# Performance work log

Hardware: AMD Instinct MI355X
Metric: run time of the kernel (lower is better)

The kernel has to match this reference:

```python
import jax, jax.numpy as jnp
import numpy as np

B, N, V, H = 8, 2048, 256, 1024
EPS = 1e-5
NEG = -1e9


def _layernorm(x, g, b):
    m = jnp.mean(x, axis=-1, keepdims=True)
    v = jnp.mean((x - m) ** 2, axis=-1, keepdims=True)
    return (x - m) / jnp.sqrt(v + EPS) * g + b


def setup_inputs() -> dict:
    key = jax.random.key(0)
    ks = jax.random.split(key, 10)
    tril = jnp.tril(jnp.ones((N, N), jnp.float32))
    return {
        "h": jax.random.normal(ks[0], (B, N, V), jnp.float32),
        "mask_one": tril,                      # keep causal entries
        "mask_zero": NEG * (1.0 - tril),       # -inf-ish above diagonal
        "ln_attn_g": jnp.ones((V,), jnp.float32),
        "ln_attn_b": jnp.zeros((V,), jnp.float32),
        "ln_mlp_g": jnp.ones((V,), jnp.float32),
        "ln_mlp_b": jnp.zeros((V,), jnp.float32),
        "wv": jax.random.normal(ks[1], (V,), jnp.float32),
        "wv_bos": jax.random.normal(ks[2], (V,), jnp.float32),
        "wo_w": jax.random.normal(ks[3], (V, V), jnp.float32) / np.sqrt(V),
        "qk_bos": jax.random.normal(ks[4], (V,), jnp.float32),
        "qk_previous": jax.random.normal(ks[5], (V,), jnp.float32),
        "qk_direction": jnp.ones((V,), jnp.float32),  # middel_layer=False, frozen
        "w1": jax.random.normal(ks[6], (H, V), jnp.float32) / np.sqrt(V),
        "w2": jax.random.normal(ks[7], (V, H), jnp.float32) / np.sqrt(H),
    }


def reference(h, mask_one, mask_zero, ln_attn_g, ln_attn_b, ln_mlp_g, ln_mlp_b,
              wv, wv_bos, wo_w, qk_bos, qk_previous, qk_direction, w1, w2):
    b, n, v = h.shape
    # mask blends LayerNorm only into row 0 (BOS position)
    attn_input = h.at[:, 0, :].set(_layernorm(h[:, 0, :], ln_attn_g, ln_attn_b))
    # value states: diag(wv) on positions 1.., wo(wv_bos) at position 0
    values = attn_input[:, 1:, :] * wv                      # [B, N-1, V]
    v_bos = wo_w @ wv_bos                                   # Linear(bias=False)
    values = jnp.concatenate(
        [jnp.broadcast_to(v_bos, (b, 1, v)), values], axis=1)  # [B, N, V]
    # sparse QK logits: column 0 term + sub-diagonal term, densified then masked
    col0 = (attn_input @ qk_bos) * (attn_input[:, 0, :] @ qk_direction)[:, None]  # [B, N]
    d = attn_input @ qk_previous                            # [B, N]
    qk = jnp.zeros((b, n, n), h.dtype).at[:, :, 0].add(col0)
    idx = jnp.arange(1, n)
    qk = qk.at[:, idx, idx - 1].add(d[:, 1:])               # row r, col r-1 = d[:, r]
    qk = qk * mask_one + mask_zero
    attn_out = jax.nn.softmax(qk, axis=-1) @ values         # [B, N, V]
    # FFN branch with its own BOS-only LayerNorm blend
    mlp_input = h.at[:, 0, :].set(_layernorm(h[:, 0, :], ln_mlp_g, ln_mlp_b))
    mlp_out = jax.nn.relu(mlp_input @ w1.T) @ w2.T          # [B, N, V]
    return attn_out + mlp_out
```

## Files before the change

### kernel.cpp

```cpp
#include <hip/hip_runtime.h>
#include <hip/hip_bf16.h>

#define BB 8
#define NN 2048
#define VV 256
#define HH 1024
#define CHK 64
#define RPC 32
constexpr float EPS = 1e-5f;

typedef __attribute__((ext_vector_type(4))) float floatx4;
typedef __attribute__((ext_vector_type(8))) short short8;

__device__ __forceinline__ void load_lds16(const void* g, void* l) {
    __builtin_amdgcn_global_load_lds((const __attribute__((address_space(1))) void*)g,
                                     (__attribute__((address_space(3))) void*)l, 16, 0, 0);
}
__device__ __forceinline__ float bf16s_to_f(short s) {
    unsigned u = ((unsigned)(unsigned short)s) << 16;
    return __builtin_bit_cast(float, u);
}

__global__ void prep_kernel(const float* __restrict__ h,
                            const float* __restrict__ g_attn, const float* __restrict__ b_attn,
                            const float* __restrict__ g_mlp,  const float* __restrict__ b_mlp,
                            const float* __restrict__ qk_dir,
                            const float* __restrict__ wo_w,  const float* __restrict__ wv_bos,
                            float* __restrict__ attn_row0, float* __restrict__ mlp_row0,
                            float* __restrict__ v_bos, float* __restrict__ sum0)
{
    int t = threadIdx.x;
    __shared__ float red[VV];
    if (blockIdx.x < BB) {
        int b = blockIdx.x;
        float x = h[(size_t)b * NN * VV + t];
        red[t] = x; __syncthreads();
        for (int s = 128; s > 0; s >>= 1) { if (t < s) red[t] += red[t + s]; __syncthreads(); }
        float m = red[0] * (1.0f / VV); __syncthreads();
        float xc = x - m;
        red[t] = xc * xc; __syncthreads();
        for (int s = 128; s > 0; s >>= 1) { if (t < s) red[t] += red[t + s]; __syncthreads(); }
        float var = red[0] * (1.0f / VV); __syncthreads();
        float inv = 1.0f / sqrtf(var + EPS);
        float an = xc * inv * g_attn[t] + b_attn[t];
        float mn = xc * inv * g_mlp[t] + b_mlp[t];
        attn_row0[b * VV + t] = an;
        mlp_row0[b * VV + t]  = mn;
        red[t] = an * qk_dir[t]; __syncthreads();
        for (int s = 128; s > 0; s >>= 1) { if (t < s) red[t] += red[t + s]; __syncthreads(); }
        if (t == 0) sum0[b] = red[0];
    } else {
        const float4* wp = reinterpret_cast<const float4*>(wo_w + (size_t)t * VV);
        const float4* vp = reinterpret_cast<const float4*>(wv_bos);
        float acc = 0.f;
        for (int j = 0; j < VV / 4; ++j) {
            float4 a = wp[j], b = vp[j];
            acc += a.x * b.x + a.y * b.y + a.z * b.z + a.w * b.w;
        }
        v_bos[t] = acc;
    }
}

__global__ __launch_bounds__(256) void scan_qkw_cvt_kernel(
    const float* __restrict__ h, const float* __restrict__ mlp_row0,
    const float* __restrict__ wv,
    const float* __restrict__ qk_bos, const float* __restrict__ qk_prev,
    const float* __restrict__ sum0,
    short* __restrict__ Xb,
    float* __restrict__ w0, float* __restrict__ wprev, float* __restrict__ wz,
    float* __restrict__ chunkSum)
{
    __shared__ float lds[4][VV];
    int wave = threadIdx.x >> 6, lane = threadIdx.x & 63;
    int b = blockIdx.x / CHK, c = blockIdx.x % CHK;
    int r0 = c * RPC + wave * 8;
    float4 wv4 = reinterpret_cast<const float4*>(wv)[lane];
    float4 qb4 = reinterpret_cast<const float4*>(qk_bos)[lane];
    float4 qp4 = reinterpret_cast<const float4*>(qk_prev)[lane];
    float s0b = sum0[b];
    float4 vsum = {0.f, 0.f, 0.f, 0.f};
#pragma unroll
    for (int rr = 0; rr < 8; ++rr) {
        int r = r0 + rr;
        size_t base = ((size_t)b * NN + r) * VV;
        float4 x = *reinterpret_cast<const float4*>(h + base + lane * 4);
        float4 xs = x;
        if (r == 0) xs = *reinterpret_cast<const float4*>(mlp_row0 + b * VV + lane * 4);
        __hip_bfloat16 c0 = __float2bfloat16(xs.x), c1 = __float2bfloat16(xs.y),
                       c2 = __float2bfloat16(xs.z), c3 = __float2bfloat16(xs.w);
        short4 pk;
        pk.x = *reinterpret_cast<short*>(&c0);
        pk.y = *reinterpret_cast<short*>(&c1);
        pk.z = *reinterpret_cast<short*>(&c2);
        pk.w = *reinterpret_cast<short*>(&c3);
        *reinterpret_cast<short4*>(Xb + base + lane * 4) = pk;
        if (r != 0) {
            vsum.x += bf16s_to_f(pk.x) * wv4.x; vsum.y += bf16s_to_f(pk.y) * wv4.y;
            vsum.z += bf16s_to_f(pk.z) * wv4.z; vsum.w += bf16s_to_f(pk.w) * wv4.w;
        }
        float s1 = x.x * qb4.x + x.y * qb4.y + x.z * qb4.z + x.w * qb4.w;
        float s2 = x.x * qp4.x + x.y * qp4.y + x.z * qp4.z + x.w * qp4.w;
        for (int off = 32; off > 0; off >>= 1) {
            s1 += __shfl_down(s1, off);
            s2 += __shfl_down(s2, off);
        }
        if (lane == 0) {
            int gid = b * NN + r;
            float W0, WP, WZ;
            if (r == 0) { W0 = 1.f; WP = 0.f; WZ = 0.f; }
            else if (r == 1) {
                float a = s1 * s0b + s2;
                float m = fmaxf(a, 0.f);
                float ea = expf(a - m), ez = expf(-m);
                float Z = ea + ez;
                W0 = ea / Z; WZ = ez / Z; WP = WZ;
            } else {
                float a = s1 * s0b;
                float m = fmaxf(fmaxf(a, s2), 0.f);
                float ea = expf(a - m), ed = expf(s2 - m), ez = expf(-m);
                float Z = ea + ed + (float)(r - 1) * ez;
                W0 = ea / Z; WP = ed / Z; WZ = ez / Z;
            }
            w0[gid] = W0; wprev[gid] = WP; wz[gid] = WZ;
        }
    }
    reinterpret_cast<float4*>(lds[wave])[lane] = vsum;
    __syncthreads();
    int v = threadIdx.x;
    chunkSum[((size_t)b * CHK + c) * VV + v] = lds[0][v] + lds[1][v] + lds[2][v] + lds[3][v];
}

__global__ void chunkscan_kernel(float* __restrict__ chunkSum)
{
    int b = blockIdx.x, v = threadIdx.x;
    float vals[CHK];
#pragma unroll
    for (int c = 0; c < CHK; ++c) vals[c] = chunkSum[(b * CHK + c) * VV + v];
    float run = 0.f;
#pragma unroll
    for (int c = 0; c < CHK; ++c) { float t = vals[c]; vals[c] = run; run += t; }
#pragma unroll
    for (int c = 0; c < CHK; ++c) chunkSum[(b * CHK + c) * VV + v] = vals[c];
}

__global__ __launch_bounds__(128) void attn_kernel(
    const short* __restrict__ Xb, const float* __restrict__ wv,
    const float* __restrict__ v_bos,
    const float* __restrict__ w0, const float* __restrict__ wprev,
    const float* __restrict__ wz, const float* __restrict__ chunkSum,
    float* __restrict__ out)
{
    int b = blockIdx.x / CHK, c = blockIdx.x % CHK;
    int v = threadIdx.x * 2;
    float2 wv2 = *reinterpret_cast<const float2*>(wv + v);
    float2 vb2 = *reinterpret_cast<const float2*>(v_bos + v);
    float2 S = *reinterpret_cast<const float2*>(chunkSum + (b * CHK + c) * VV + v);
    int r0 = c * RPC;
    float2 prev = {0.f, 0.f};
    if (r0 > 0) {
        short2 p = *reinterpret_cast<const short2*>(Xb + ((size_t)b * NN + r0 - 1) * VV + v);
        prev.x = bf16s_to_f(p.x) * wv2.x; prev.y = bf16s_to_f(p.y) * wv2.y;
    }
    for (int r = r0; r < r0 + RPC; ++r) {
        size_t idx = ((size_t)b * NN + r) * VV + v;
        float2 o;
        if (r == 0) {
            o = vb2;
            prev.x = 0.f; prev.y = 0.f;
        } else {
            short2 xv = *reinterpret_cast<const short2*>(Xb + idx);
            float2 val;
            val.x = bf16s_to_f(xv.x) * wv2.x; val.y = bf16s_to_f(xv.y) * wv2.y;
            S.x += val.x; S.y += val.y;
            int wi = b * NN + r;
            float W0 = w0[wi], WD = wprev[wi] - wz[wi], WZ = wz[wi];
            o.x = W0 * vb2.x + WD * prev.x + WZ * S.x;
            o.y = W0 * vb2.y + WD * prev.y + WZ * S.y;
            prev = val;
        }
        *reinterpret_cast<float2*>(out + idx) = o;
    }
}

__global__ void cvt_w_kernel(const float* __restrict__ w1, const float* __restrict__ w2,
                             __hip_bfloat16* __restrict__ w1b, __hip_bfloat16* __restrict__ w2b)
{
    int i = (blockIdx.x * blockDim.x + threadIdx.x) * 4;
    const float* src;
    __hip_bfloat16* dst;
    if (i < HH * VV) { src = w1 + i; dst = w1b + i; }
    else             { src = w2 + (i - HH * VV); dst = w2b + (i - HH * VV); }
    float4 x = *reinterpret_cast<const float4*>(src);
    dst[0] = __float2bfloat16(x.x);
    dst[1] = __float2bfloat16(x.y);
    dst[2] = __float2bfloat16(x.z);
    dst[3] = __float2bfloat16(x.w);
}

__global__ __launch_bounds__(512) void mlp_fused3(const short* __restrict__ Xb,
                                                  const short* __restrict__ w1b,
                                                  const short* __restrict__ w2b,
                                                  float* __restrict__ out)
{
    __shared__ __align__(16) short sW1[2][64 * 256];
    __shared__ __align__(16) short sW2[2][256 * 64];
    __shared__ __align__(16) short sY[64 * 64];
    int wave = threadIdx.x >> 6, lane = threadIdx.x & 63;
    int wm = wave >> 2, wn = wave & 3;
    int ra = lane & 15, q = lane >> 4;
    int m0 = blockIdx.x * 64;

    short8 xf[8][2];
#pragma unroll
    for (int ks = 0; ks < 8; ++ks)
#pragma unroll
        for (int i = 0; i < 2; ++i)
            xf[ks][i] = *reinterpret_cast<const short8*>(
                Xb + (size_t)(m0 + wm * 32 + i * 16 + ra) * VV + ks * 32 + q * 8);

    floatx4 oacc[2][4];
#pragma unroll
    for (int i = 0; i < 2; ++i)
#pragma unroll
        for (int j = 0; j < 4; ++j) oacc[i][j] = floatx4{0.f, 0.f, 0.f, 0.f};

    auto stage = [&](int hc, int buf) {
#pragma unroll
        for (int it = 0; it < 4; ++it) {
            int g = wave * 4 + it;
            int n = g * 2 + (lane >> 5);
            int slot = lane & 31;
            load_lds16(w1b + (size_t)(hc * 64 + n) * VV + (slot ^ (n & 7)) * 8,
                       &sW1[buf][g * 512]);
        }
#pragma unroll
        for (int it = 0; it < 4; ++it) {
            int g = wave * 4 + it;
            int v = g * 8 + (lane >> 3);
            int slot = lane & 7;
            load_lds16(w2b + (size_t)v * HH + hc * 64 + (slot ^ (v & 7)) * 8,
                       &sW2[buf][g * 512]);
        }
    };

    stage(0, 0);
    for (int hc = 0; hc < 16; ++hc) {
        int p = hc & 1;
        __syncthreads();
        if (hc < 15) stage(hc + 1, p ^ 1);

        floatx4 yacc[2];
        yacc[0] = floatx4{0.f, 0.f, 0.f, 0.f};
        yacc[1] = floatx4{0.f, 0.f, 0.f, 0.f};
        int nb = wn * 16 + ra;
#pragma unroll
        for (int ks = 0; ks < 8; ++ks) {
            short8 bfr = *reinterpret_cast<const short8*>(
                &sW1[p][nb * 256 + (((ks * 4 + q) ^ (ra & 7)) * 8)]);
#pragma unroll
            for (int i = 0; i < 2; ++i)
                yacc[i] = __builtin_amdgcn_mfma_f32_16x16x32_bf16(xf[ks][i], bfr, yacc[i], 0, 0, 0);
        }
#pragma unroll
        for (int i = 0; i < 2; ++i)
#pragma unroll
            for (int reg = 0; reg < 4; ++reg) {
                int m = wm * 32 + i * 16 + q * 4 + reg;
                int ke = wn * 16 + ra;
                __hip_bfloat16 hb = __float2bfloat16(fmaxf(yacc[i][reg], 0.f));
                sY[m * 64 + (((ke >> 3) ^ (m & 7)) * 8) + (ke & 7)] =
                    *reinterpret_cast<short*>(&hb);
            }
        __syncthreads();

#pragma unroll
        for (int kk = 0; kk < 2; ++kk) {
            short8 a2[2];
#pragma unroll
            for (int i = 0; i < 2; ++i) {
                int m = wm * 32 + i * 16 + ra;
                a2[i] = *reinterpret_cast<const short8*>(
                    &sY[m * 64 + (((kk * 4 + q) ^ (ra & 7)) * 8)]);
            }
#pragma unroll
            for (int j = 0; j < 4; ++j) {
                int v = wn * 64 + j * 16 + ra;
                short8 b2 = *reinterpret_cast<const short8*>(
                    &sW2[p][v * 64 + (((kk * 4 + q) ^ (ra & 7)) * 8)]);
#pragma unroll
                for (int i = 0; i < 2; ++i)
                    oacc[i][j] = __builtin_amdgcn_mfma_f32_16x16x32_bf16(a2[i], b2, oacc[i][j], 0, 0, 0);
            }
        }
    }

#pragma unroll
    for (int i = 0; i < 2; ++i)
#pragma unroll
        for (int j = 0; j < 4; ++j)
#pragma unroll
            for (int reg = 0; reg < 4; ++reg) {
                int row = m0 + wm * 32 + i * 16 + q * 4 + reg;
                int col = wn * 64 + j * 16 + ra;
                out[(size_t)row * VV + col] += oacc[i][j][reg];
            }
}

extern "C" void kernel_launch(void* const* d_in, const int* in_sizes, int n_in,
                              void* d_out, int out_size, void* d_ws, size_t ws_size,
                              hipStream_t stream)
{
    const float* h        = (const float*)d_in[0];
    const float* ln_attn_g = (const float*)d_in[3];
    const float* ln_attn_b = (const float*)d_in[4];
    const float* ln_mlp_g  = (const float*)d_in[5];
    const float* ln_mlp_b  = (const float*)d_in[6];
    const float* wv        = (const float*)d_in[7];
    const float* wv_bos    = (const float*)d_in[8];
    const float* wo_w      = (const float*)d_in[9];
    const float* qk_bos    = (const float*)d_in[10];
    const float* qk_prev   = (const float*)d_in[11];
    const float* qk_dir    = (const float*)d_in[12];
    const float* w1        = (const float*)d_in[13];
    const float* w2        = (const float*)d_in[14];
    float* out = (float*)d_out;

    float* attn_row0 = (float*)d_ws;
    float* mlp_row0  = attn_row0 + BB * VV;
    float* v_bos     = mlp_row0 + BB * VV;
    float* sum0      = v_bos + VV;
    float* w0        = sum0 + 8;
    float* wprev     = w0 + BB * NN;
    float* wzz       = wprev + BB * NN;
    float* chunkSum  = wzz + BB * NN;
    short* Xb            = (short*)(chunkSum + BB * CHK * VV);
    __hip_bfloat16* w1b  = (__hip_bfloat16*)(Xb + (size_t)BB * NN * VV);
    __hip_bfloat16* w2b  = w1b + HH * VV;

    prep_kernel<<<BB + 1, 256, 0, stream>>>(h, ln_attn_g, ln_attn_b, ln_mlp_g, ln_mlp_b,
                                            qk_dir, wo_w, wv_bos,
                                            attn_row0, mlp_row0, v_bos, sum0);
    cvt_w_kernel<<<(2 * HH * VV / 4) / 256, 256, 0, stream>>>(w1, w2, w1b, w2b);
    scan_qkw_cvt_kernel<<<BB * CHK, 256, 0, stream>>>(h, mlp_row0, wv, qk_bos, qk_prev,
                                                      sum0, Xb, w0, wprev, wzz, chunkSum);
    chunkscan_kernel<<<BB, 256, 0, stream>>>(chunkSum);
    attn_kernel<<<BB * CHK, 128, 0, stream>>>(Xb, wv, v_bos, w0, wprev, wzz, chunkSum, out);
    mlp_fused3<<<256, 512, 0, stream>>>(Xb, (const short*)w1b, (const short*)w2b, out);
}
```

Baseline: 172.3 us.

## Merge weight conversion into prep, drop chunk scan kernel, restructure MLP to 4 waves

Weight bf16 conversion is folded into the prep kernel as extra blocks, and the separate chunk-scan kernel is removed: each attention block now sums its preceding chunk totals itself. The MLP kernel moves from 8 waves to 4 waves per block, with each wave covering all 64 rows and doubling its accumulator tiles. The next-chunk weight staging is issued after the first GEMM's barrier instead of before it. These cut launch count and per-block synchronisation, at the cost of redundant prefix reads in the attention kernel and higher register pressure in the MLP.

```diff
diff --git a/kernel.cpp b/kernel.cpp
--- a/kernel.cpp
+++ b/kernel.cpp
@@ -21,15 +21,30 @@
     return __builtin_bit_cast(float, u);
 }
 
-__global__ void prep_kernel(const float* __restrict__ h,
-                            const float* __restrict__ g_attn, const float* __restrict__ b_attn,
-                            const float* __restrict__ g_mlp,  const float* __restrict__ b_mlp,
-                            const float* __restrict__ qk_dir,
-                            const float* __restrict__ wo_w,  const float* __restrict__ wv_bos,
-                            float* __restrict__ attn_row0, float* __restrict__ mlp_row0,
-                            float* __restrict__ v_bos, float* __restrict__ sum0)
+__global__ void prep_cvt_kernel(const float* __restrict__ h,
+                                const float* __restrict__ g_attn, const float* __restrict__ b_attn,
+                                const float* __restrict__ g_mlp,  const float* __restrict__ b_mlp,
+                                const float* __restrict__ qk_dir,
+                                const float* __restrict__ wo_w,  const float* __restrict__ wv_bos,
+                                const float* __restrict__ w1, const float* __restrict__ w2,
+                                float* __restrict__ attn_row0, float* __restrict__ mlp_row0,
+                                float* __restrict__ v_bos, float* __restrict__ sum0,
+                                __hip_bfloat16* __restrict__ w1b, __hip_bfloat16* __restrict__ w2b)
 {
     int t = threadIdx.x;
+    if (blockIdx.x > BB) {
+        int i = ((blockIdx.x - BB - 1) * 256 + t) * 4;
+        const float* src;
+        __hip_bfloat16* dst;
+        if (i < HH * VV) { src = w1 + i; dst = w1b + i; }
+        else             { src = w2 + (i - HH * VV); dst = w2b + (i - HH * VV); }
+        float4 x = *reinterpret_cast<const float4*>(src);
+        dst[0] = __float2bfloat16(x.x);
+        dst[1] = __float2bfloat16(x.y);
+        dst[2] = __float2bfloat16(x.z);
+        dst[3] = __float2bfloat16(x.w);
+        return;
+    }
     __shared__ float red[VV];
     if (blockIdx.x < BB) {
         int b = blockIdx.x;
@@ -130,19 +145,6 @@
     chunkSum[((size_t)b * CHK + c) * VV + v] = lds[0][v] + lds[1][v] + lds[2][v] + lds[3][v];
 }
 
-__global__ void chunkscan_kernel(float* __restrict__ chunkSum)
-{
-    int b = blockIdx.x, v = threadIdx.x;
-    float vals[CHK];
-#pragma unroll
-    for (int c = 0; c < CHK; ++c) vals[c] = chunkSum[(b * CHK + c) * VV + v];
-    float run = 0.f;
-#pragma unroll
-    for (int c = 0; c < CHK; ++c) { float t = vals[c]; vals[c] = run; run += t; }
-#pragma unroll
-    for (int c = 0; c < CHK; ++c) chunkSum[(b * CHK + c) * VV + v] = vals[c];
-}
-
 __global__ __launch_bounds__(128) void attn_kernel(
     const short* __restrict__ Xb, const float* __restrict__ wv,
     const float* __restrict__ v_bos,
@@ -154,7 +156,11 @@
     int v = threadIdx.x * 2;
     float2 wv2 = *reinterpret_cast<const float2*>(wv + v);
     float2 vb2 = *reinterpret_cast<const float2*>(v_bos + v);
-    float2 S = *reinterpret_cast<const float2*>(chunkSum + (b * CHK + c) * VV + v);
+    float2 S = {0.f, 0.f};
+    for (int cc = 0; cc < c; ++cc) {
+        float2 t = *reinterpret_cast<const float2*>(chunkSum + (b * CHK + cc) * VV + v);
+        S.x += t.x; S.y += t.y;
+    }
     int r0 = c * RPC;
     float2 prev = {0.f, 0.f};
     if (r0 > 0) {
@@ -182,63 +188,47 @@
     }
 }
 
-__global__ void cvt_w_kernel(const float* __restrict__ w1, const float* __restrict__ w2,
-                             __hip_bfloat16* __restrict__ w1b, __hip_bfloat16* __restrict__ w2b)
-{
-    int i = (blockIdx.x * blockDim.x + threadIdx.x) * 4;
-    const float* src;
-    __hip_bfloat16* dst;
-    if (i < HH * VV) { src = w1 + i; dst = w1b + i; }
-    else             { src = w2 + (i - HH * VV); dst = w2b + (i - HH * VV); }
-    float4 x = *reinterpret_cast<const float4*>(src);
-    dst[0] = __float2bfloat16(x.x);
-    dst[1] = __float2bfloat16(x.y);
-    dst[2] = __float2bfloat16(x.z);
-    dst[3] = __float2bfloat16(x.w);
-}
-
-__global__ __launch_bounds__(512) void mlp_fused3(const short* __restrict__ Xb,
-                                                  const short* __restrict__ w1b,
-                                                  const short* __restrict__ w2b,
-                                                  float* __restrict__ out)
+__global__ __launch_bounds__(256, 1) void mlp_fused4(const short* __restrict__ Xb,
+                                                     const short* __restrict__ w1b,
+                                                     const short* __restrict__ w2b,
+                                                     float* __restrict__ out)
 {
     __shared__ __align__(16) short sW1[2][64 * 256];
     __shared__ __align__(16) short sW2[2][256 * 64];
     __shared__ __align__(16) short sY[64 * 64];
     int wave = threadIdx.x >> 6, lane = threadIdx.x & 63;
-    int wm = wave >> 2, wn = wave & 3;
     int ra = lane & 15, q = lane >> 4;
     int m0 = blockIdx.x * 64;
 
-    short8 xf[8][2];
+    short8 xf[8][4];
 #pragma unroll
     for (int ks = 0; ks < 8; ++ks)
 #pragma unroll
-        for (int i = 0; i < 2; ++i)
+        for (int i = 0; i < 4; ++i)
             xf[ks][i] = *reinterpret_cast<const short8*>(
-                Xb + (size_t)(m0 + wm * 32 + i * 16 + ra) * VV + ks * 32 + q * 8);
-
-    floatx4 oacc[2][4];
-#pragma unroll
-    for (int i = 0; i < 2; ++i)
+                Xb + (size_t)(m0 + i * 16 + ra) * VV + ks * 32 + q * 8);
+
+    floatx4 oacc[4][4];
+#pragma unroll
+    for (int i = 0; i < 4; ++i)
 #pragma unroll
         for (int j = 0; j < 4; ++j) oacc[i][j] = floatx4{0.f, 0.f, 0.f, 0.f};
 
     auto stage = [&](int hc, int buf) {
 #pragma unroll
-        for (int it = 0; it < 4; ++it) {
-            int g = wave * 4 + it;
+        for (int it = 0; it < 8; ++it) {
+            int g = wave * 8 + it;
             int n = g * 2 + (lane >> 5);
             int slot = lane & 31;
-            load_lds16(w1b + (size_t)(hc * 64 + n) * VV + (slot ^ (n & 7)) * 8,
+            load_lds16(w1b + (size_t)(hc * 64 + n) * VV + ((slot ^ (n & 7)) * 8),
                        &sW1[buf][g * 512]);
         }
 #pragma unroll
-        for (int it = 0; it < 4; ++it) {
-            int g = wave * 4 + it;
+        for (int it = 0; it < 8; ++it) {
+            int g = wave * 8 + it;
             int v = g * 8 + (lane >> 3);
             int slot = lane & 7;
-            load_lds16(w2b + (size_t)v * HH + hc * 64 + (slot ^ (v & 7)) * 8,
+            load_lds16(w2b + (size_t)v * HH + hc * 64 + ((slot ^ (v & 7)) * 8),
                        &sW2[buf][g * 512]);
         }
     };
@@ -247,61 +237,62 @@
     for (int hc = 0; hc < 16; ++hc) {
         int p = hc & 1;
         __syncthreads();
-        if (hc < 15) stage(hc + 1, p ^ 1);
-
-        floatx4 yacc[2];
-        yacc[0] = floatx4{0.f, 0.f, 0.f, 0.f};
-        yacc[1] = floatx4{0.f, 0.f, 0.f, 0.f};
-        int nb = wn * 16 + ra;
+
+        floatx4 yacc[4];
+#pragma unroll
+        for (int i = 0; i < 4; ++i) yacc[i] = floatx4{0.f, 0.f, 0.f, 0.f};
+        int nb = wave * 16 + ra;
 #pragma unroll
         for (int ks = 0; ks < 8; ++ks) {
             short8 bfr = *reinterpret_cast<const short8*>(
-                &sW1[p][nb * 256 + (((ks * 4 + q) ^ (ra & 7)) * 8)]);
-#pragma unroll
-            for (int i = 0; i < 2; ++i)
+                &sW1[p][nb * 256 + (((ks * 4 + q) ^ (nb & 7)) * 8)]);
+#pragma unroll
+            for (int i = 0; i < 4; ++i)
                 yacc[i] = __builtin_amdgcn_mfma_f32_16x16x32_bf16(xf[ks][i], bfr, yacc[i], 0, 0, 0);
         }
 #pragma unroll
-        for (int i = 0; i < 2; ++i)
+        for (int i = 0; i < 4; ++i)
 #pragma unroll
             for (int reg = 0; reg < 4; ++reg) {
-                int m = wm * 32 + i * 16 + q * 4 + reg;
-                int ke = wn * 16 + ra;
+                int m = i * 16 + q * 4 + reg;
+                int ke = wave * 16 + ra;
                 __hip_bfloat16 hb = __float2bfloat16(fmaxf(yacc[i][reg], 0.f));
                 sY[m * 64 + (((ke >> 3) ^ (m & 7)) * 8) + (ke & 7)] =
                     *reinterpret_cast<short*>(&hb);
             }
         __syncthreads();
 
+        if (hc < 15) stage(hc + 1, p ^ 1);
+
 #pragma unroll
         for (int kk = 0; kk < 2; ++kk) {
-            short8 a2[2];
-#pragma unroll
-            for (int i = 0; i < 2; ++i) {
-                int m = wm * 32 + i * 16 + ra;
+            short8 a2[4];
+#pragma unroll
+            for (int i = 0; i < 4; ++i) {
+                int m = i * 16 + ra;
                 a2[i] = *reinterpret_cast<const short8*>(
-                    &sY[m * 64 + (((kk * 4 + q) ^ (ra & 7)) * 8)]);
+                    &sY[m * 64 + (((kk * 4 + q) ^ (m & 7)) * 8)]);
             }
 #pragma unroll
             for (int j = 0; j < 4; ++j) {
-                int v = wn * 64 + j * 16 + ra;
+                int v = wave * 64 + j * 16 + ra;
                 short8 b2 = *reinterpret_cast<const short8*>(
-                    &sW2[p][v * 64 + (((kk * 4 + q) ^ (ra & 7)) * 8)]);
-#pragma unroll
-                for (int i = 0; i < 2; ++i)
+                    &sW2[p][v * 64 + (((kk * 4 + q) ^ (v & 7)) * 8)]);
+#pragma unroll
+                for (int i = 0; i < 4; ++i)
                     oacc[i][j] = __builtin_amdgcn_mfma_f32_16x16x32_bf16(a2[i], b2, oacc[i][j], 0, 0, 0);
             }
         }
     }
 
 #pragma unroll
-    for (int i = 0; i < 2; ++i)
+    for (int i = 0; i < 4; ++i)
 #pragma unroll
         for (int j = 0; j < 4; ++j)
 #pragma unroll
             for (int reg = 0; reg < 4; ++reg) {
-                int row = m0 + wm * 32 + i * 16 + q * 4 + reg;
-                int col = wn * 64 + j * 16 + ra;
+                int row = m0 + i * 16 + q * 4 + reg;
+                int col = wave * 64 + j * 16 + ra;
                 out[(size_t)row * VV + col] += oacc[i][j][reg];
             }
 }
@@ -337,13 +328,11 @@
     __hip_bfloat16* w1b  = (__hip_bfloat16*)(Xb + (size_t)BB * NN * VV);
     __hip_bfloat16* w2b  = w1b + HH * VV;
 
-    prep_kernel<<<BB + 1, 256, 0, stream>>>(h, ln_attn_g, ln_attn_b, ln_mlp_g, ln_mlp_b,
-                                            qk_dir, wo_w, wv_bos,
-                                            attn_row0, mlp_row0, v_bos, sum0);
-    cvt_w_kernel<<<(2 * HH * VV / 4) / 256, 256, 0, stream>>>(w1, w2, w1b, w2b);
+    prep_cvt_kernel<<<BB + 1 + (2 * HH * VV / 4) / 256, 256, 0, stream>>>(
+        h, ln_attn_g, ln_attn_b, ln_mlp_g, ln_mlp_b, qk_dir, wo_w, wv_bos,
+        w1, w2, attn_row0, mlp_row0, v_bos, sum0, w1b, w2b);
     scan_qkw_cvt_kernel<<<BB * CHK, 256, 0, stream>>>(h, mlp_row0, wv, qk_bos, qk_prev,
                                                       sum0, Xb, w0, wprev, wzz, chunkSum);
-    chunkscan_kernel<<<BB, 256, 0, stream>>>(chunkSum);
     attn_kernel<<<BB * CHK, 128, 0, stream>>>(Xb, wv, v_bos, w0, wprev, wzz, chunkSum, out);
-    mlp_fused3<<<256, 512, 0, stream>>>(Xb, (const short*)w1b, (const short*)w2b, out);
-}
+    mlp_fused4<<<256, 256, 0, stream>>>(Xb, (const short*)w1b, (const short*)w2b, out);
+}
```

Measured after the change: 194.5 us. 1.13x slower.

## Merge prep and weight-convert kernels, drop chunk scan, single-buffer MLP LDS

Applied to the files above, without the earlier changes.

Folds the weight bf16 conversion into the prep kernel as extra blocks, and removes the separate chunk-prefix-scan kernel. Each attention block now sums the preceding chunk totals itself, and row 0 is written outside the loop so the loop body has no branch. The MLP kernel drops double-buffered LDS staging for a single buffer with load-then-sync, which cuts LDS use (possibly raising occupancy) but exposes load latency. The aim is fewer launches and less launch overhead, at the cost of redundant prefix sums and lost load/compute overlap.

```diff
diff --git a/kernel.cpp b/kernel.cpp
--- a/kernel.cpp
+++ b/kernel.cpp
@@ -21,15 +21,30 @@
     return __builtin_bit_cast(float, u);
 }
 
-__global__ void prep_kernel(const float* __restrict__ h,
-                            const float* __restrict__ g_attn, const float* __restrict__ b_attn,
-                            const float* __restrict__ g_mlp,  const float* __restrict__ b_mlp,
-                            const float* __restrict__ qk_dir,
-                            const float* __restrict__ wo_w,  const float* __restrict__ wv_bos,
-                            float* __restrict__ attn_row0, float* __restrict__ mlp_row0,
-                            float* __restrict__ v_bos, float* __restrict__ sum0)
+__global__ void prep_cvt_kernel(const float* __restrict__ h,
+                                const float* __restrict__ g_attn, const float* __restrict__ b_attn,
+                                const float* __restrict__ g_mlp,  const float* __restrict__ b_mlp,
+                                const float* __restrict__ qk_dir,
+                                const float* __restrict__ wo_w,  const float* __restrict__ wv_bos,
+                                const float* __restrict__ w1, const float* __restrict__ w2,
+                                float* __restrict__ attn_row0, float* __restrict__ mlp_row0,
+                                float* __restrict__ v_bos, float* __restrict__ sum0,
+                                __hip_bfloat16* __restrict__ w1b, __hip_bfloat16* __restrict__ w2b)
 {
     int t = threadIdx.x;
+    if (blockIdx.x > BB) {
+        int i = ((blockIdx.x - BB - 1) * 256 + t) * 4;
+        const float* src;
+        __hip_bfloat16* dst;
+        if (i < HH * VV) { src = w1 + i; dst = w1b + i; }
+        else             { src = w2 + (i - HH * VV); dst = w2b + (i - HH * VV); }
+        float4 x = *reinterpret_cast<const float4*>(src);
+        dst[0] = __float2bfloat16(x.x);
+        dst[1] = __float2bfloat16(x.y);
+        dst[2] = __float2bfloat16(x.z);
+        dst[3] = __float2bfloat16(x.w);
+        return;
+    }
     __shared__ float red[VV];
     if (blockIdx.x < BB) {
         int b = blockIdx.x;
@@ -130,19 +145,6 @@
     chunkSum[((size_t)b * CHK + c) * VV + v] = lds[0][v] + lds[1][v] + lds[2][v] + lds[3][v];
 }
 
-__global__ void chunkscan_kernel(float* __restrict__ chunkSum)
-{
-    int b = blockIdx.x, v = threadIdx.x;
-    float vals[CHK];
-#pragma unroll
-    for (int c = 0; c < CHK; ++c) vals[c] = chunkSum[(b * CHK + c) * VV + v];
-    float run = 0.f;
-#pragma unroll
-    for (int c = 0; c < CHK; ++c) { float t = vals[c]; vals[c] = run; run += t; }
-#pragma unroll
-    for (int c = 0; c < CHK; ++c) chunkSum[(b * CHK + c) * VV + v] = vals[c];
-}
-
 __global__ __launch_bounds__(128) void attn_kernel(
     const short* __restrict__ Xb, const float* __restrict__ wv,
     const float* __restrict__ v_bos,
@@ -154,56 +156,46 @@
     int v = threadIdx.x * 2;
     float2 wv2 = *reinterpret_cast<const float2*>(wv + v);
     float2 vb2 = *reinterpret_cast<const float2*>(v_bos + v);
-    float2 S = *reinterpret_cast<const float2*>(chunkSum + (b * CHK + c) * VV + v);
+    float2 S = {0.f, 0.f};
+    for (int cc = 0; cc < c; ++cc) {
+        float2 t = *reinterpret_cast<const float2*>(chunkSum + (b * CHK + cc) * VV + v);
+        S.x += t.x; S.y += t.y;
+    }
     int r0 = c * RPC;
+    int rstart = r0;
     float2 prev = {0.f, 0.f};
-    if (r0 > 0) {
+    if (c == 0) {
+        *reinterpret_cast<float2*>(out + (size_t)b * NN * VV + v) = vb2;
+        rstart = 1;
+    } else {
         short2 p = *reinterpret_cast<const short2*>(Xb + ((size_t)b * NN + r0 - 1) * VV + v);
         prev.x = bf16s_to_f(p.x) * wv2.x; prev.y = bf16s_to_f(p.y) * wv2.y;
     }
-    for (int r = r0; r < r0 + RPC; ++r) {
+    int rend = r0 + RPC;
+#pragma unroll 4
+    for (int r = rstart; r < rend; ++r) {
         size_t idx = ((size_t)b * NN + r) * VV + v;
+        short2 xv = *reinterpret_cast<const short2*>(Xb + idx);
+        float2 val;
+        val.x = bf16s_to_f(xv.x) * wv2.x; val.y = bf16s_to_f(xv.y) * wv2.y;
+        S.x += val.x; S.y += val.y;
+        int wi = b * NN + r;
+        float W0 = w0[wi], WD = wprev[wi] - wz[wi], WZ = wz[wi];
         float2 o;
-        if (r == 0) {
-            o = vb2;
-            prev.x = 0.f; prev.y = 0.f;
-        } else {
-            short2 xv = *reinterpret_cast<const short2*>(Xb + idx);
-            float2 val;
-            val.x = bf16s_to_f(xv.x) * wv2.x; val.y = bf16s_to_f(xv.y) * wv2.y;
-            S.x += val.x; S.y += val.y;
-            int wi = b * NN + r;
-            float W0 = w0[wi], WD = wprev[wi] - wz[wi], WZ = wz[wi];
-            o.x = W0 * vb2.x + WD * prev.x + WZ * S.x;
-            o.y = W0 * vb2.y + WD * prev.y + WZ * S.y;
-            prev = val;
-        }
+        o.x = W0 * vb2.x + WD * prev.x + WZ * S.x;
+        o.y = W0 * vb2.y + WD * prev.y + WZ * S.y;
+        prev = val;
         *reinterpret_cast<float2*>(out + idx) = o;
     }
 }
 
-__global__ void cvt_w_kernel(const float* __restrict__ w1, const float* __restrict__ w2,
-                             __hip_bfloat16* __restrict__ w1b, __hip_bfloat16* __restrict__ w2b)
-{
-    int i = (blockIdx.x * blockDim.x + threadIdx.x) * 4;
-    const float* src;
-    __hip_bfloat16* dst;
-    if (i < HH * VV) { src = w1 + i; dst = w1b + i; }
-    else             { src = w2 + (i - HH * VV); dst = w2b + (i - HH * VV); }
-    float4 x = *reinterpret_cast<const float4*>(src);
-    dst[0] = __float2bfloat16(x.x);
-    dst[1] = __float2bfloat16(x.y);
-    dst[2] = __float2bfloat16(x.z);
-    dst[3] = __float2bfloat16(x.w);
-}
-
-__global__ __launch_bounds__(512) void mlp_fused3(const short* __restrict__ Xb,
+__global__ __launch_bounds__(512) void mlp_fused5(const short* __restrict__ Xb,
                                                   const short* __restrict__ w1b,
                                                   const short* __restrict__ w2b,
                                                   float* __restrict__ out)
 {
-    __shared__ __align__(16) short sW1[2][64 * 256];
-    __shared__ __align__(16) short sW2[2][256 * 64];
+    __shared__ __align__(16) short sW1[64 * 256];
+    __shared__ __align__(16) short sW2[256 * 64];
     __shared__ __align__(16) short sY[64 * 64];
     int wave = threadIdx.x >> 6, lane = threadIdx.x & 63;
     int wm = wave >> 2, wn = wave & 3;
@@ -224,30 +216,25 @@
 #pragma unroll
         for (int j = 0; j < 4; ++j) oacc[i][j] = floatx4{0.f, 0.f, 0.f, 0.f};
 
-    auto stage = [&](int hc, int buf) {
+    for (int hc = 0; hc < 16; ++hc) {
+        __syncthreads();
 #pragma unroll
         for (int it = 0; it < 4; ++it) {
             int g = wave * 4 + it;
             int n = g * 2 + (lane >> 5);
             int slot = lane & 31;
-            load_lds16(w1b + (size_t)(hc * 64 + n) * VV + (slot ^ (n & 7)) * 8,
-                       &sW1[buf][g * 512]);
+            load_lds16(w1b + (size_t)(hc * 64 + n) * VV + ((slot ^ (n & 7)) * 8),
+                       sW1 + g * 512);
         }
 #pragma unroll
         for (int it = 0; it < 4; ++it) {
             int g = wave * 4 + it;
             int v = g * 8 + (lane >> 3);
             int slot = lane & 7;
-            load_lds16(w2b + (size_t)v * HH + hc * 64 + (slot ^ (v & 7)) * 8,
-                       &sW2[buf][g * 512]);
-        }
-    };
-
-    stage(0, 0);
-    for (int hc = 0; hc < 16; ++hc) {
-        int p = hc & 1;
+            load_lds16(w2b + (size_t)v * HH + hc * 64 + ((slot ^ (v & 7)) * 8),
+                       sW2 + g * 512);
+        }
         __syncthreads();
-        if (hc < 15) stage(hc + 1, p ^ 1);
 
         floatx4 yacc[2];
         yacc[0] = floatx4{0.f, 0.f, 0.f, 0.f};
@@ -256,7 +243,7 @@
 #pragma unroll
         for (int ks = 0; ks < 8; ++ks) {
             short8 bfr = *reinterpret_cast<const short8*>(
-                &sW1[p][nb * 256 + (((ks * 4 + q) ^ (ra & 7)) * 8)]);
+                &sW1[nb * 256 + (((ks * 4 + q) ^ (ra & 7)) * 8)]);
 #pragma unroll
             for (int i = 0; i < 2; ++i)
                 yacc[i] = __builtin_amdgcn_mfma_f32_16x16x32_bf16(xf[ks][i], bfr, yacc[i], 0, 0, 0);
@@ -286,7 +273,7 @@
             for (int j = 0; j < 4; ++j) {
                 int v = wn * 64 + j * 16 + ra;
                 short8 b2 = *reinterpret_cast<const short8*>(
-                    &sW2[p][v * 64 + (((kk * 4 + q) ^ (ra & 7)) * 8)]);
+                    &sW2[v * 64 + (((kk * 4 + q) ^ (ra & 7)) * 8)]);
 #pragma unroll
                 for (int i = 0; i < 2; ++i)
                     oacc[i][j] = __builtin_amdgcn_mfma_f32_16x16x32_bf16(a2[i], b2, oacc[i][j], 0, 0, 0);
@@ -337,13 +324,12 @@
     __hip_bfloat16* w1b  = (__hip_bfloat16*)(Xb + (size_t)BB * NN * VV);
     __hip_bfloat16* w2b  = w1b + HH * VV;
 
-    prep_kernel<<<BB + 1, 256, 0, stream>>>(h, ln_attn_g, ln_attn_b, ln_mlp_g, ln_mlp_b,
-                                            qk_dir, wo_w, wv_bos,
-                                            attn_row0, mlp_row0, v_bos, sum0);
-    cvt_w_kernel<<<(2 * HH * VV / 4) / 256, 256, 0, stream>>>(w1, w2, w1b, w2b);
+    prep_cvt_kernel<<<BB + 1 + (2 * HH * VV / 4) / 256, 256, 0, stream>>>(
+        h, ln_attn_g, ln_attn_b, ln_mlp_g, ln_mlp_b, qk_dir, wo_w, wv_bos,
+        w1, w2, attn_row0, mlp_row0, v_bos, sum0, w1b, w2b);
     scan_qkw_cvt_kernel<<<BB * CHK, 256, 0, stream>>>(h, mlp_row0, wv, qk_bos, qk_prev,
                                                       sum0, Xb, w0, wprev, wzz, chunkSum);
-    chunkscan_kernel<<<BB, 256, 0, stream>>>(chunkSum);
     attn_kernel<<<BB * CHK, 128, 0, stream>>>(Xb, wv, v_bos, w0, wprev, wzz, chunkSum, out);
-    mlp_fused3<<<256, 512, 0, stream>>>(Xb, (const short*)w1b, (const short*)w2b, out);
-}
+    mlp_fused5<<<256, 512, 0, stream>>>((const short*)Xb, (const short*)w1b,
+                                        (const short*)w2b, out);
+}
```

Result: slower. 187.3 us (+8.7%).
